# Optimization experiments

Hardware: AMD Instinct MI355X
Metric: run time of the kernel (lower is better)

Reference implementation:

```python
import jax, jax.numpy as jnp
import numpy as np

EMB_DIM = 512
N_HEAD = 8
HEAD_DIM = EMB_DIM // N_HEAD
SEQ_LEN = 2048
BATCH = 4


def setup_inputs() -> dict:
    key = jax.random.key(0)
    k1, k2, k3 = jax.random.split(key, 3)
    emb = jax.random.normal(k1, (SEQ_LEN, BATCH, EMB_DIM), dtype=jnp.float32)
    # torch Linear weight layout: (out_features, in_features)
    W = jax.random.normal(k2, (3 * EMB_DIM, EMB_DIM), dtype=jnp.float32) * 0.02
    b = jax.random.normal(k3, (3 * EMB_DIM,), dtype=jnp.float32) * 0.02
    return {"emb": emb, "W": W, "b": b}


def reference(emb, W, b):
    L, B, E = emb.shape
    scaling = (E / N_HEAD) ** -0.5
    # qkv projection: (L, B, 3E)
    ft = jnp.einsum('lbe,oe->lbo', emb, W) + b
    # interleaved per-head qkv split, matching reshape(L, B*nh, -1).chunk(3, -1)
    ft = ft.reshape(L, B * N_HEAD, 3 * HEAD_DIM).transpose(1, 0, 2)  # (B*nh, L, 3*hd)
    q, k, v = jnp.split(ft, 3, axis=-1)  # each (B*nh, L, hd)
    # attention scores with value-based zero mask
    scores = jnp.einsum('bld,bmd->blm', q, k) * scaling  # (B*nh, L, L)
    mask = scores == 0
    scores = jnp.where(mask, -jnp.inf, scores)
    attn = jax.nn.softmax(scores, axis=-1)
    attn = jnp.where(mask, jnp.zeros((), attn.dtype), attn)
    out = jnp.einsum('blm,bmd->bld', attn, v)  # (B*nh, L, hd)
    out = out.transpose(1, 0, 2).reshape(L, B, E)
    return out
```

## Files before the change

kernel.cpp:

```cpp
#include <hip/hip_runtime.h>
#include <hip/hip_bf16.h>
#include <cstdint>
#include <math.h>


typedef __bf16 bf16x8 __attribute__((ext_vector_type(8)));
typedef float  f32x4  __attribute__((ext_vector_type(4)));
typedef float  f32x16 __attribute__((ext_vector_type(16)));
typedef unsigned int uint32x4 __attribute__((ext_vector_type(4)));

#define MFMA16(a, b, c) __builtin_amdgcn_mfma_f32_16x16x32_bf16(a, b, c, 0, 0, 0)
#define MFMA32(a, b, c) __builtin_amdgcn_mfma_f32_32x32x16_bf16(a, b, c, 0, 0, 0)

#define EXP2F(x) __builtin_amdgcn_exp2f(x)

#define QSCALE 0.18033688011112042f

enum {
  LSEQ = 2048,
  NBATCH = 4,
  EMB = 512,
  NHEAD = 8,
  HDIM = 64,
  NBH = NBATCH * NHEAD,
  MROWS = LSEQ * NBATCH,
  KDIM = EMB,
  NOUT = 3 * EMB
};

__device__ inline void gload_lds16(const void* g, void* l) {
  __builtin_amdgcn_global_load_lds(
      (__attribute__((address_space(1))) void*)(uintptr_t)g,
      (__attribute__((address_space(3))) void*)(uint32_t)(uintptr_t)l,
      16, 0, 0);
}

__device__ inline unsigned packbf(float a, float b) {
  unsigned short ua = __builtin_bit_cast(unsigned short, (__bf16)a);
  unsigned short ub = __builtin_bit_cast(unsigned short, (__bf16)b);
  return (unsigned)ua | ((unsigned)ub << 16);
}

__device__ inline bf16x8 frag_from(unsigned w0, unsigned w1, unsigned w2, unsigned w3) {
  uint32x4 v = {w0, w1, w2, w3};
  return __builtin_bit_cast(bf16x8, v);
}

__global__ __launch_bounds__(256) void cvt2_kernel(const float* __restrict__ a,
                                                   __bf16* __restrict__ oa, int na8,
                                                   const float* __restrict__ b,
                                                   __bf16* __restrict__ ob, int nb8) {
  int i = blockIdx.x * 256 + threadIdx.x;
  const float* in;
  __bf16* out;
  int idx;
  if (i < na8) {
    in = a; out = oa; idx = i;
  } else {
    idx = i - na8;
    if (idx >= nb8) return;
    in = b; out = ob;
  }
  const float4* p = (const float4*)in + (size_t)idx * 2;
  float4 x = p[0], y = p[1];
  bf16x8 o;
  o[0] = (__bf16)x.x; o[1] = (__bf16)x.y; o[2] = (__bf16)x.z; o[3] = (__bf16)x.w;
  o[4] = (__bf16)y.x; o[5] = (__bf16)y.y; o[6] = (__bf16)y.z; o[7] = (__bf16)y.w;
  *(bf16x8*)(out + (size_t)idx * 8) = o;
}

__global__ __launch_bounds__(256) void qkv_gemm_kernel(
    const __bf16* __restrict__ A, const __bf16* __restrict__ Bt,
    const float* __restrict__ bias,
    __bf16* __restrict__ Qh, __bf16* __restrict__ Kh, __bf16* __restrict__ Vth) {
  __shared__ __align__(16) __bf16 As[2][128 * 64];
  __shared__ __align__(16) __bf16 Bs[2][128 * 64];

  const int tid = threadIdx.x;
  const int wid = tid >> 6, lane = tid & 63;
  const int g = lane >> 4, lx = lane & 15;

  const int orig = blockIdx.x;
  const int xcd = orig & 7, rr = orig >> 3;
  const int mt_local = rr / 12;
  const int ntile = rr - mt_local * 12;
  const int mtile = xcd * 8 + mt_local;
  const int b = mtile >> 4;
  const int l0 = (mtile & 15) * 128;

  const int wm = (wid >> 1) * 64, wn = (wid & 1) * 64;
  const int lr = lane >> 3;
  const int ch = (lane & 7) ^ lr;

  const int rowB0 = ntile * 128;

#define GSTAGE(bufi, ks)                                                          \
  {                                                                               \
    _Pragma("unroll") for (int i = 0; i < 4; ++i) {                               \
      const int chunk = wid * 4 + i;                                              \
      gload_lds16(A + ((size_t)(l0 + chunk * 8 + lr) * NBATCH + b) * KDIM +       \
                      (ks) * 64 + ch * 8,                                         \
                  &As[bufi][chunk * 512]);                                        \
      gload_lds16(Bt + (size_t)(rowB0 + chunk * 8 + lr) * KDIM + (ks) * 64 +      \
                      ch * 8,                                                     \
                  &Bs[bufi][chunk * 512]);                                        \
    }                                                                             \
  }

  f32x4 acc[4][4] = {};

  GSTAGE(0, 0);
  __syncthreads();

  for (int k = 0; k < 8; ++k) {
    const int cur = k & 1;
    if (k < 7) GSTAGE(cur ^ 1, k + 1);
#pragma unroll
    for (int kk = 0; kk < 2; ++kk) {
      bf16x8 af[4], bfr[4];
#pragma unroll
      for (int t = 0; t < 4; ++t)
        af[t] = *(const bf16x8*)&As[cur][(wm + t * 16 + lx) * 64 +
                                         (((kk * 4 + g) ^ (lx & 7)) << 3)];
#pragma unroll
      for (int t = 0; t < 4; ++t)
        bfr[t] = *(const bf16x8*)&Bs[cur][(wn + t * 16 + lx) * 64 +
                                          (((kk * 4 + g) ^ (lx & 7)) << 3)];
#pragma unroll
      for (int mi = 0; mi < 4; ++mi)
#pragma unroll
        for (int ni = 0; ni < 4; ++ni)
          acc[mi][ni] = MFMA16(af[mi], bfr[ni], acc[mi][ni]);
    }
    __syncthreads();
  }
#undef GSTAGE

#pragma unroll
  for (int ni = 0; ni < 4; ++ni) {
    int o = ntile * 128 + wn + ni * 16 + lx;
    float bv = bias[o];
    unsigned h = (unsigned)o / 192u;
    unsigned w = (unsigned)o - h * 192u;
    const size_t bh = (size_t)(b * NHEAD) + h;
#pragma unroll
    for (int mi = 0; mi < 4; ++mi) {
      const int l = l0 + wm + mi * 16 + g * 4;
      if (w < 64u) {
#pragma unroll
        for (int r = 0; r < 4; ++r)
          Qh[(bh * LSEQ + l + r) * HDIM + w] =
              (__bf16)((acc[mi][ni][r] + bv) * QSCALE);
      } else if (w < 128u) {
#pragma unroll
        for (int r = 0; r < 4; ++r)
          Kh[(bh * LSEQ + l + r) * HDIM + (w - 64u)] = (__bf16)(acc[mi][ni][r] + bv);
      } else {
        unsigned u0 = packbf(acc[mi][ni][0] + bv, acc[mi][ni][1] + bv);
        unsigned u1 = packbf(acc[mi][ni][2] + bv, acc[mi][ni][3] + bv);
        uint2 uv = make_uint2(u0, u1);
        *(uint2*)&Vth[(bh * HDIM + (w - 128u)) * LSEQ + l] = uv;
      }
    }
  }
}

__global__ __launch_bounds__(512, 2) void attn_kernel(const __bf16* __restrict__ Qh,
                                                      const __bf16* __restrict__ Kh,
                                                      const __bf16* __restrict__ Vth,
                                                      float* __restrict__ out) {
  __shared__ __align__(16) __bf16 Ks[4][64 * 64];
  __shared__ __align__(16) __bf16 Vs[4][64 * 64];

  const int flat = blockIdx.x;
  const int sw = (flat & 7) * 64 + (flat >> 3);
  const int bh = sw >> 4, qt = sw & 15;
  const int tid = threadIdx.x, wid = tid >> 6, lane = tid & 63;
  const int pair = wid >> 1, role = wid & 1;
  const int ql = lane & 31, hi = lane >> 5;
  const int rb = ql & 7;

  const __bf16* Kb = Kh + (size_t)bh * (LSEQ * HDIM);
  const __bf16* Vb = Vth + (size_t)bh * (HDIM * LSEQ);

  const __bf16* Qp =
      Qh + ((size_t)bh * LSEQ + qt * 128 + pair * 32 + ql) * HDIM + hi * 8;
  bf16x8 qf[4];
#pragma unroll
  for (int s = 0; s < 4; ++s) qf[s] = *(const bf16x8*)(Qp + s * 16);

  const int lr3 = lane >> 3;
  const int ch = (lane & 7) ^ lr3;

#define STAGE_T(tt)                                                        \
  {                                                                        \
    const int tn_ = (tt) & 31;                                             \
    const int b_ = tn_ & 3;                                                \
    gload_lds16(Kb + (size_t)(tn_ * 64 + wid * 8 + lr3) * HDIM + ch * 8,   \
                &Ks[b_][(wid * 8) * 64]);                                  \
    gload_lds16(Vb + (size_t)(wid * 8 + lr3) * LSEQ + tn_ * 64 + ch * 8,   \
                &Vs[b_][(wid * 8) * 64]);                                  \
  }

  int ko[4], vo[4];
#pragma unroll
  for (int fs = 0; fs < 4; ++fs)
    ko[fs] = (role * 32 + ql) * 64 + (((2 * fs + hi) ^ rb) << 3);
#pragma unroll
  for (int dt = 0; dt < 2; ++dt)
#pragma unroll
    for (int ks = 0; ks < 2; ++ks)
      vo[dt * 2 + ks] =
          (dt * 32 + ql) * 64 + (((role * 4 + 2 * ks + hi) ^ rb) << 3);

  f32x16 ot[2] = {};
  float lacc[8] = {};
  bf16x8 pfA[2], pfB[2];

#define HEAD                                           \
  asm volatile("s_waitcnt vmcnt(2)" ::: "memory");     \
  __builtin_amdgcn_s_barrier();                        \
  asm volatile("" ::: "memory");

#define FILL(pfX, s_)                                                        \
  {                                                                          \
    const int cur_ = (s_) & 3;                                               \
    const __bf16* kr_ = &Ks[cur_][0];                                        \
    bf16x8 k0 = *(const bf16x8*)(kr_ + ko[0]);                               \
    bf16x8 k1 = *(const bf16x8*)(kr_ + ko[1]);                               \
    bf16x8 k2 = *(const bf16x8*)(kr_ + ko[2]);                               \
    bf16x8 k3 = *(const bf16x8*)(kr_ + ko[3]);                               \
    f32x16 st_ = {};                                                         \
    __builtin_amdgcn_s_setprio(1);                                           \
    st_ = MFMA32(k0, qf[0], st_);                                            \
    st_ = MFMA32(k1, qf[1], st_);                                            \
    st_ = MFMA32(k2, qf[2], st_);                                            \
    st_ = MFMA32(k3, qf[3], st_);                                            \
    __builtin_amdgcn_s_setprio(0);                                           \
    _Pragma("unroll") for (int r = 0; r < 16; ++r) {                         \
      float e_ = EXP2F(st_[r]);                                              \
      st_[r] = e_;                                                           \
      lacc[r & 7] += e_;                                                     \
    }                                                                        \
    unsigned b0 = packbf(st_[0], st_[1]), b1 = packbf(st_[2], st_[3]);       \
    unsigned b2 = packbf(st_[4], st_[5]), b3 = packbf(st_[6], st_[7]);       \
    unsigned b4 = packbf(st_[8], st_[9]), b5 = packbf(st_[10], st_[11]);     \
    unsigned b6 = packbf(st_[12], st_[13]), b7 = packbf(st_[14], st_[15]);   \
    asm("v_permlane32_swap_b32 %0, %1" : "+v"(b0), "+v"(b2));                \
    asm("v_permlane32_swap_b32 %0, %1" : "+v"(b1), "+v"(b3));                \
    asm("v_permlane32_swap_b32 %0, %1" : "+v"(b4), "+v"(b6));                \
    asm("v_permlane32_swap_b32 %0, %1" : "+v"(b5), "+v"(b7));                \
    pfX[0] = frag_from(b0, b1, b2, b3);                                      \
    pfX[1] = frag_from(b4, b5, b6, b7);                                      \
  }

#define PVSTEP(pfX, bidx)                                  \
  {                                                        \
    const __bf16* vr_ = &Vs[bidx][0];                      \
    bf16x8 v0 = *(const bf16x8*)(vr_ + vo[0]);             \
    bf16x8 v1 = *(const bf16x8*)(vr_ + vo[1]);             \
    bf16x8 v2 = *(const bf16x8*)(vr_ + vo[2]);             \
    bf16x8 v3 = *(const bf16x8*)(vr_ + vo[3]);             \
    __builtin_amdgcn_s_setprio(1);                         \
    ot[0] = MFMA32(v0, pfX[0], ot[0]);                     \
    ot[0] = MFMA32(v1, pfX[1], ot[0]);                     \
    ot[1] = MFMA32(v2, pfX[0], ot[1]);                     \
    ot[1] = MFMA32(v3, pfX[1], ot[1]);                     \
    __builtin_amdgcn_s_setprio(0);                         \
  }

  STAGE_T(0);
  STAGE_T(1);

  HEAD;
  FILL(pfA, 0);
  STAGE_T(2);

  HEAD;
  FILL(pfB, 1);
  PVSTEP(pfA, 0);
  STAGE_T(3);

  for (int i = 0; i < 15; ++i) {
    const int s0 = 2 + 2 * i;
    HEAD;
    FILL(pfA, s0);
    PVSTEP(pfB, (s0 - 1) & 3);
    STAGE_T(s0 + 2);
    HEAD;
    FILL(pfB, s0 + 1);
    PVSTEP(pfA, s0 & 3);
    STAGE_T(s0 + 3);
  }
  PVSTEP(pfB, 3);

#undef STAGE_T
#undef HEAD
#undef FILL
#undef PVSTEP

  float ls = 0.f;
#pragma unroll
  for (int r = 0; r < 8; ++r) ls += lacc[r];
  ls += __shfl_xor(ls, 32);

  asm volatile("s_waitcnt vmcnt(0) lgkmcnt(0)" ::: "memory");
  __syncthreads();
  float* stash_ot = (float*)&Ks[0][0];
  float* stash_ls = (float*)&Vs[0][0];
  float* myo = stash_ot + (wid * 64 + lane) * 16;
  f32x16 give = role ? ot[0] : ot[1];
#pragma unroll
  for (int g4 = 0; g4 < 4; ++g4) {
    float4 v4 = make_float4(give[4 * g4 + 0], give[4 * g4 + 1],
                            give[4 * g4 + 2], give[4 * g4 + 3]);
    *(float4*)(myo + 4 * g4) = v4;
  }
  stash_ls[wid * 64 + lane] = ls;
  __syncthreads();

  const float* po = stash_ot + ((wid ^ 1) * 64 + lane) * 16;
  f32x16 mine = role ? ot[1] : ot[0];
#pragma unroll
  for (int r = 0; r < 16; ++r) mine[r] += po[r];
  const float lst = ls + stash_ls[(wid ^ 1) * 64 + lane];
  const float inv = 1.f / lst;

  const int lq = qt * 128 + pair * 32 + ql;
  float* ob = out + (size_t)lq * (NBATCH * EMB) + (bh >> 3) * EMB + (bh & 7) * HDIM;
#pragma unroll
  for (int g4 = 0; g4 < 4; ++g4) {
    float4 v4 = make_float4(mine[4 * g4 + 0] * inv, mine[4 * g4 + 1] * inv,
                            mine[4 * g4 + 2] * inv, mine[4 * g4 + 3] * inv);
    *(float4*)(ob + role * 32 + g4 * 8 + hi * 4) = v4;
  }
}

extern "C" void kernel_launch(void* const* d_in, const int* in_sizes, int n_in,
                              void* d_out, int out_size, void* d_ws, size_t ws_size,
                              hipStream_t stream) {
  const float* emb = (const float*)d_in[0];
  const float* W = (const float*)d_in[1];
  const float* bias = (const float*)d_in[2];
  float* out = (float*)d_out;

  char* ws = (char*)d_ws;
  __bf16* embh = (__bf16*)(ws);
  __bf16* Wh   = (__bf16*)(ws + 8388608);
  __bf16* Qh   = (__bf16*)(ws + 9961472);
  __bf16* Kh   = (__bf16*)(ws + 18350080);
  __bf16* Vth  = (__bf16*)(ws + 26738688);

  const int na8 = MROWS * KDIM / 8;
  const int nb8 = NOUT * KDIM / 8;
  cvt2_kernel<<<dim3((na8 + nb8 + 255) / 256), dim3(256), 0, stream>>>(
      emb, embh, na8, W, Wh, nb8);
  qkv_gemm_kernel<<<dim3(768), dim3(256), 0, stream>>>(
      embh, Wh, bias, Qh, Kh, Vth);
  attn_kernel<<<dim3(NBH * (LSEQ / 128)), dim3(512), 0, stream>>>(Qh, Kh, Vth, out);
}
```

Before: 80.58 us.

## Process two KV tiles per barrier instead of software-pipelined FILL/PVSTEP

Replaces the staggered pipeline, where the QK/softmax of one 64-key tile overlapped the PV of the previous tile with one barrier per tile, with a loop that handles two tiles per iteration. Each iteration runs QK for both tiles, then exp, then PV for both, and then stages the next two tiles after a second barrier. This halves the barrier count per tile pair and interleaves independent MFMA chains to expose ILP. In exchange it gives up the cross-tile overlap of exp with PV MFMAs, and the staging slots are only refilled after both tiles are consumed.

```diff
diff --git a/kernel.cpp b/kernel.cpp
--- a/kernel.cpp
+++ b/kernel.cpp
@@ -214,94 +214,97 @@
           (dt * 32 + ql) * 64 + (((role * 4 + 2 * ks + hi) ^ rb) << 3);
 
   f32x16 ot[2] = {};
-  float lacc[8] = {};
-  bf16x8 pfA[2], pfB[2];
-
-#define HEAD                                           \
-  asm volatile("s_waitcnt vmcnt(2)" ::: "memory");     \
-  __builtin_amdgcn_s_barrier();                        \
-  asm volatile("" ::: "memory");
-
-#define FILL(pfX, s_)                                                        \
-  {                                                                          \
-    const int cur_ = (s_) & 3;                                               \
-    const __bf16* kr_ = &Ks[cur_][0];                                        \
-    bf16x8 k0 = *(const bf16x8*)(kr_ + ko[0]);                               \
-    bf16x8 k1 = *(const bf16x8*)(kr_ + ko[1]);                               \
-    bf16x8 k2 = *(const bf16x8*)(kr_ + ko[2]);                               \
-    bf16x8 k3 = *(const bf16x8*)(kr_ + ko[3]);                               \
-    f32x16 st_ = {};                                                         \
-    __builtin_amdgcn_s_setprio(1);                                           \
-    st_ = MFMA32(k0, qf[0], st_);                                            \
-    st_ = MFMA32(k1, qf[1], st_);                                            \
-    st_ = MFMA32(k2, qf[2], st_);                                            \
-    st_ = MFMA32(k3, qf[3], st_);                                            \
-    __builtin_amdgcn_s_setprio(0);                                           \
-    _Pragma("unroll") for (int r = 0; r < 16; ++r) {                         \
-      float e_ = EXP2F(st_[r]);                                              \
-      st_[r] = e_;                                                           \
-      lacc[r & 7] += e_;                                                     \
-    }                                                                        \
-    unsigned b0 = packbf(st_[0], st_[1]), b1 = packbf(st_[2], st_[3]);       \
-    unsigned b2 = packbf(st_[4], st_[5]), b3 = packbf(st_[6], st_[7]);       \
-    unsigned b4 = packbf(st_[8], st_[9]), b5 = packbf(st_[10], st_[11]);     \
-    unsigned b6 = packbf(st_[12], st_[13]), b7 = packbf(st_[14], st_[15]);   \
-    asm("v_permlane32_swap_b32 %0, %1" : "+v"(b0), "+v"(b2));                \
-    asm("v_permlane32_swap_b32 %0, %1" : "+v"(b1), "+v"(b3));                \
-    asm("v_permlane32_swap_b32 %0, %1" : "+v"(b4), "+v"(b6));                \
-    asm("v_permlane32_swap_b32 %0, %1" : "+v"(b5), "+v"(b7));                \
-    pfX[0] = frag_from(b0, b1, b2, b3);                                      \
-    pfX[1] = frag_from(b4, b5, b6, b7);                                      \
-  }
-
-#define PVSTEP(pfX, bidx)                                  \
-  {                                                        \
-    const __bf16* vr_ = &Vs[bidx][0];                      \
-    bf16x8 v0 = *(const bf16x8*)(vr_ + vo[0]);             \
-    bf16x8 v1 = *(const bf16x8*)(vr_ + vo[1]);             \
-    bf16x8 v2 = *(const bf16x8*)(vr_ + vo[2]);             \
-    bf16x8 v3 = *(const bf16x8*)(vr_ + vo[3]);             \
-    __builtin_amdgcn_s_setprio(1);                         \
-    ot[0] = MFMA32(v0, pfX[0], ot[0]);                     \
-    ot[0] = MFMA32(v1, pfX[1], ot[0]);                     \
-    ot[1] = MFMA32(v2, pfX[0], ot[1]);                     \
-    ot[1] = MFMA32(v3, pfX[1], ot[1]);                     \
-    __builtin_amdgcn_s_setprio(0);                         \
-  }
+  float lacc[4] = {};
 
   STAGE_T(0);
   STAGE_T(1);
-
-  HEAD;
-  FILL(pfA, 0);
   STAGE_T(2);
-
-  HEAD;
-  FILL(pfB, 1);
-  PVSTEP(pfA, 0);
   STAGE_T(3);
 
-  for (int i = 0; i < 15; ++i) {
-    const int s0 = 2 + 2 * i;
-    HEAD;
-    FILL(pfA, s0);
-    PVSTEP(pfB, (s0 - 1) & 3);
-    STAGE_T(s0 + 2);
-    HEAD;
-    FILL(pfB, s0 + 1);
-    PVSTEP(pfA, s0 & 3);
-    STAGE_T(s0 + 3);
-  }
-  PVSTEP(pfB, 3);
-
+  for (int ss = 0; ss < 16; ++ss) {
+    const int c0 = (2 * ss) & 3;
+    asm volatile("s_waitcnt vmcnt(4)" ::: "memory");
+    __builtin_amdgcn_s_barrier();
+    asm volatile("" ::: "memory");
+
+    const __bf16* krA = &Ks[c0][0];
+    const __bf16* krB = &Ks[c0 + 1][0];
+    f32x16 sa = {}, sb = {};
+    __builtin_amdgcn_s_setprio(1);
+#pragma unroll
+    for (int fs = 0; fs < 4; ++fs) {
+      bf16x8 ka = *(const bf16x8*)(krA + ko[fs]);
+      sa = MFMA32(ka, qf[fs], sa);
+      bf16x8 kb = *(const bf16x8*)(krB + ko[fs]);
+      sb = MFMA32(kb, qf[fs], sb);
+    }
+    __builtin_amdgcn_s_setprio(0);
+
+#pragma unroll
+    for (int r = 0; r < 16; ++r) {
+      float ea = EXP2F(sa[r]);
+      float eb = EXP2F(sb[r]);
+      sa[r] = ea;
+      sb[r] = eb;
+      lacc[r & 3] += ea + eb;
+    }
+
+    bf16x8 pfA0, pfA1, pfB0, pfB1;
+    {
+      unsigned a0 = packbf(sa[0], sa[1]), a1 = packbf(sa[2], sa[3]);
+      unsigned a2 = packbf(sa[4], sa[5]), a3 = packbf(sa[6], sa[7]);
+      unsigned a4 = packbf(sa[8], sa[9]), a5 = packbf(sa[10], sa[11]);
+      unsigned a6 = packbf(sa[12], sa[13]), a7 = packbf(sa[14], sa[15]);
+      asm("v_permlane32_swap_b32 %0, %1" : "+v"(a0), "+v"(a2));
+      asm("v_permlane32_swap_b32 %0, %1" : "+v"(a1), "+v"(a3));
+      asm("v_permlane32_swap_b32 %0, %1" : "+v"(a4), "+v"(a6));
+      asm("v_permlane32_swap_b32 %0, %1" : "+v"(a5), "+v"(a7));
+      pfA0 = frag_from(a0, a1, a2, a3);
+      pfA1 = frag_from(a4, a5, a6, a7);
+      unsigned b0 = packbf(sb[0], sb[1]), b1 = packbf(sb[2], sb[3]);
+      unsigned b2 = packbf(sb[4], sb[5]), b3 = packbf(sb[6], sb[7]);
+      unsigned b4 = packbf(sb[8], sb[9]), b5 = packbf(sb[10], sb[11]);
+      unsigned b6 = packbf(sb[12], sb[13]), b7 = packbf(sb[14], sb[15]);
+      asm("v_permlane32_swap_b32 %0, %1" : "+v"(b0), "+v"(b2));
+      asm("v_permlane32_swap_b32 %0, %1" : "+v"(b1), "+v"(b3));
+      asm("v_permlane32_swap_b32 %0, %1" : "+v"(b4), "+v"(b6));
+      asm("v_permlane32_swap_b32 %0, %1" : "+v"(b5), "+v"(b7));
+      pfB0 = frag_from(b0, b1, b2, b3);
+      pfB1 = frag_from(b4, b5, b6, b7);
+    }
+
+    const __bf16* vrA = &Vs[c0][0];
+    const __bf16* vrB = &Vs[c0 + 1][0];
+    __builtin_amdgcn_s_setprio(1);
+    {
+      bf16x8 v0 = *(const bf16x8*)(vrA + vo[0]);
+      bf16x8 v2 = *(const bf16x8*)(vrA + vo[2]);
+      ot[0] = MFMA32(v0, pfA0, ot[0]);
+      ot[1] = MFMA32(v2, pfA0, ot[1]);
+      bf16x8 v1 = *(const bf16x8*)(vrA + vo[1]);
+      bf16x8 v3 = *(const bf16x8*)(vrA + vo[3]);
+      ot[0] = MFMA32(v1, pfA1, ot[0]);
+      ot[1] = MFMA32(v3, pfA1, ot[1]);
+      bf16x8 w0 = *(const bf16x8*)(vrB + vo[0]);
+      bf16x8 w2 = *(const bf16x8*)(vrB + vo[2]);
+      ot[0] = MFMA32(w0, pfB0, ot[0]);
+      ot[1] = MFMA32(w2, pfB0, ot[1]);
+      bf16x8 w1 = *(const bf16x8*)(vrB + vo[1]);
+      bf16x8 w3 = *(const bf16x8*)(vrB + vo[3]);
+      ot[0] = MFMA32(w1, pfB1, ot[0]);
+      ot[1] = MFMA32(w3, pfB1, ot[1]);
+    }
+    __builtin_amdgcn_s_setprio(0);
+
+    asm volatile("" ::: "memory");
+    __builtin_amdgcn_s_barrier();
+    asm volatile("" ::: "memory");
+    STAGE_T(2 * ss + 4);
+    STAGE_T(2 * ss + 5);
+  }
 #undef STAGE_T
-#undef HEAD
-#undef FILL
-#undef PVSTEP
-
-  float ls = 0.f;
-#pragma unroll
-  for (int r = 0; r < 8; ++r) ls += lacc[r];
+
+  float ls = lacc[0] + lacc[1] + lacc[2] + lacc[3];
   ls += __shfl_xor(ls, 32);
 
   asm volatile("s_waitcnt vmcnt(0) lgkmcnt(0)" ::: "memory");
```

New measurement: 81.67 us. Within noise of the previous version (+1.4%).

## Fuse fp32-to-bf16 conversion of embeddings into QKV GEMM A-tile loading

Applied to the files above, without the earlier changes.

The GEMM now reads fp32 embeddings directly into registers, converts them to bf16, and writes them into swizzled LDS. This removes the separate conversion pass over the 16MB activation tensor and its round trip through the workspace. Only the weight matrix still goes through a standalone conversion kernel. The change adds register pressure and VALU conversion work inside the GEMM main loop, and sets launch bounds to 3 blocks per CU.

```diff
diff --git a/kernel.cpp b/kernel.cpp
--- a/kernel.cpp
+++ b/kernel.cpp
@@ -46,31 +46,21 @@
   return __builtin_bit_cast(bf16x8, v);
 }
 
-__global__ __launch_bounds__(256) void cvt2_kernel(const float* __restrict__ a,
-                                                   __bf16* __restrict__ oa, int na8,
-                                                   const float* __restrict__ b,
-                                                   __bf16* __restrict__ ob, int nb8) {
+__global__ __launch_bounds__(256) void cvtW_kernel(const float* __restrict__ in,
+                                                   __bf16* __restrict__ out,
+                                                   int n8) {
   int i = blockIdx.x * 256 + threadIdx.x;
-  const float* in;
-  __bf16* out;
-  int idx;
-  if (i < na8) {
-    in = a; out = oa; idx = i;
-  } else {
-    idx = i - na8;
-    if (idx >= nb8) return;
-    in = b; out = ob;
-  }
-  const float4* p = (const float4*)in + (size_t)idx * 2;
-  float4 x = p[0], y = p[1];
+  if (i >= n8) return;
+  const float4* p = (const float4*)in + (size_t)i * 2;
+  float4 a = p[0], b = p[1];
   bf16x8 o;
-  o[0] = (__bf16)x.x; o[1] = (__bf16)x.y; o[2] = (__bf16)x.z; o[3] = (__bf16)x.w;
-  o[4] = (__bf16)y.x; o[5] = (__bf16)y.y; o[6] = (__bf16)y.z; o[7] = (__bf16)y.w;
-  *(bf16x8*)(out + (size_t)idx * 8) = o;
-}
-
-__global__ __launch_bounds__(256) void qkv_gemm_kernel(
-    const __bf16* __restrict__ A, const __bf16* __restrict__ Bt,
+  o[0] = (__bf16)a.x; o[1] = (__bf16)a.y; o[2] = (__bf16)a.z; o[3] = (__bf16)a.w;
+  o[4] = (__bf16)b.x; o[5] = (__bf16)b.y; o[6] = (__bf16)b.z; o[7] = (__bf16)b.w;
+  *(bf16x8*)(out + (size_t)i * 8) = o;
+}
+
+__global__ __launch_bounds__(256, 3) void qkv_gemm_kernel(
+    const float* __restrict__ Af, const __bf16* __restrict__ Bt,
     const float* __restrict__ bias,
     __bf16* __restrict__ Qh, __bf16* __restrict__ Kh, __bf16* __restrict__ Vth) {
   __shared__ __align__(16) __bf16 As[2][128 * 64];
@@ -90,31 +80,60 @@
 
   const int wm = (wid >> 1) * 64, wn = (wid & 1) * 64;
   const int lr = lane >> 3;
-  const int ch = (lane & 7) ^ lr;
+  const int sc = lane & 7;
+  const int ch = sc ^ lr;
 
   const int rowB0 = ntile * 128;
 
-#define GSTAGE(bufi, ks)                                                          \
-  {                                                                               \
-    _Pragma("unroll") for (int i = 0; i < 4; ++i) {                               \
-      const int chunk = wid * 4 + i;                                              \
-      gload_lds16(A + ((size_t)(l0 + chunk * 8 + lr) * NBATCH + b) * KDIM +       \
-                      (ks) * 64 + ch * 8,                                         \
-                  &As[bufi][chunk * 512]);                                        \
-      gload_lds16(Bt + (size_t)(rowB0 + chunk * 8 + lr) * KDIM + (ks) * 64 +      \
-                      ch * 8,                                                     \
-                  &Bs[bufi][chunk * 512]);                                        \
-    }                                                                             \
+  f32x4 ra[8];
+
+#define ALOAD(ks)                                                                \
+  {                                                                              \
+    _Pragma("unroll") for (int i = 0; i < 4; ++i) {                              \
+      const int chunk = wid * 4 + i;                                             \
+      const float* src = Af + ((size_t)(l0 + chunk * 8 + lr) * NBATCH + b) *     \
+                                  KDIM + (ks) * 64 + sc * 8;                     \
+      ra[2 * i] = *(const f32x4*)src;                                            \
+      ra[2 * i + 1] = *(const f32x4*)(src + 4);                                  \
+    }                                                                            \
+  }
+
+#define AWRITE(bufi)                                                             \
+  {                                                                              \
+    _Pragma("unroll") for (int i = 0; i < 4; ++i) {                              \
+      const int chunk = wid * 4 + i;                                             \
+      uint32x4 wv;                                                               \
+      wv[0] = packbf(ra[2 * i][0], ra[2 * i][1]);                                \
+      wv[1] = packbf(ra[2 * i][2], ra[2 * i][3]);                                \
+      wv[2] = packbf(ra[2 * i + 1][0], ra[2 * i + 1][1]);                        \
+      wv[3] = packbf(ra[2 * i + 1][2], ra[2 * i + 1][3]);                        \
+      *(uint32x4*)&As[bufi][chunk * 512 + lr * 64 + (ch << 3)] = wv;             \
+    }                                                                            \
+  }
+
+#define BSTAGE(bufi, ks)                                                         \
+  {                                                                              \
+    _Pragma("unroll") for (int i = 0; i < 4; ++i) {                              \
+      const int chunk = wid * 4 + i;                                             \
+      gload_lds16(Bt + (size_t)(rowB0 + chunk * 8 + lr) * KDIM + (ks) * 64 +     \
+                      ch * 8,                                                    \
+                  &Bs[bufi][chunk * 512]);                                       \
+    }                                                                            \
   }
 
   f32x4 acc[4][4] = {};
 
-  GSTAGE(0, 0);
+  ALOAD(0);
+  BSTAGE(0, 0);
+  AWRITE(0);
   __syncthreads();
 
   for (int k = 0; k < 8; ++k) {
     const int cur = k & 1;
-    if (k < 7) GSTAGE(cur ^ 1, k + 1);
+    if (k < 7) {
+      ALOAD(k + 1);
+      BSTAGE(cur ^ 1, k + 1);
+    }
 #pragma unroll
     for (int kk = 0; kk < 2; ++kk) {
       bf16x8 af[4], bfr[4];
@@ -132,9 +151,12 @@
         for (int ni = 0; ni < 4; ++ni)
           acc[mi][ni] = MFMA16(af[mi], bfr[ni], acc[mi][ni]);
     }
+    if (k < 7) AWRITE(cur ^ 1);
     __syncthreads();
   }
-#undef GSTAGE
+#undef ALOAD
+#undef AWRITE
+#undef BSTAGE
 
 #pragma unroll
   for (int ni = 0; ni < 4; ++ni) {
@@ -345,17 +367,14 @@
   float* out = (float*)d_out;
 
   char* ws = (char*)d_ws;
-  __bf16* embh = (__bf16*)(ws);
   __bf16* Wh   = (__bf16*)(ws + 8388608);
   __bf16* Qh   = (__bf16*)(ws + 9961472);
   __bf16* Kh   = (__bf16*)(ws + 18350080);
   __bf16* Vth  = (__bf16*)(ws + 26738688);
 
-  const int na8 = MROWS * KDIM / 8;
   const int nb8 = NOUT * KDIM / 8;
-  cvt2_kernel<<<dim3((na8 + nb8 + 255) / 256), dim3(256), 0, stream>>>(
-      emb, embh, na8, W, Wh, nb8);
+  cvtW_kernel<<<dim3(nb8 / 256), dim3(256), 0, stream>>>(W, Wh, nb8);
   qkv_gemm_kernel<<<dim3(768), dim3(256), 0, stream>>>(
-      embh, Wh, bias, Qh, Kh, Vth);
+      emb, Wh, bias, Qh, Kh, Vth);
   attn_kernel<<<dim3(NBH * (LSEQ / 128)), dim3(512), 0, stream>>>(Qh, Kh, Vth, out);
 }
```

Measured after the change: 88.01 us. 1.09x slower.
